# Kernel tuning notes

Hardware: AMD Instinct MI355X
Metric: run time of the kernel (lower is better)

Reference implementation:

```python
import jax, jax.numpy as jnp
import numpy as np

N_NODES = 100000
N_EDGES = 1600000
D_IN, D_H, D_OUT = 128, 128, 64


def gcn_conv(x, src, dst, W, b, n_nodes):
    """PyG GCNConv (eval): x' = D^{-1/2} (A+I) D^{-1/2} X W + b.
    src/dst already include self-loops."""
    h = x @ W  # [N, d_out] -- transform first (fewer FLOPs when d_out <= d_in)
    deg = jax.ops.segment_sum(jnp.ones_like(dst, dtype=h.dtype), dst, num_segments=n_nodes)
    dinv = jnp.where(deg > 0, jax.lax.rsqrt(deg), 0.0)
    norm = dinv[src] * dinv[dst]  # [E]
    msg = h[src] * norm[:, None]  # gather + scale
    out = jax.ops.segment_sum(msg, dst, num_segments=n_nodes)  # scatter-add
    return out + b


def setup_inputs() -> dict:
    key = jax.random.key(0)
    k = jax.random.split(key, 8)
    x = jax.random.normal(k[0], (N_NODES, D_IN), dtype=jnp.float32)
    edge_index = jax.random.randint(k[1], (2, N_EDGES), 0, N_NODES, dtype=jnp.int32)
    s = 0.1
    W1 = jax.random.normal(k[2], (D_IN, D_H), dtype=jnp.float32) * s
    b1 = jnp.zeros((D_H,), dtype=jnp.float32)
    W2 = jax.random.normal(k[3], (D_H, D_H), dtype=jnp.float32) * s
    b2 = jnp.zeros((D_H,), dtype=jnp.float32)
    W3 = jax.random.normal(k[4], (D_H, D_OUT), dtype=jnp.float32) * s
    b3 = jnp.zeros((D_OUT,), dtype=jnp.float32)
    return {"x": x, "edge_index": edge_index, "W1": W1, "b1": b1,
            "W2": W2, "b2": b2, "W3": W3, "b3": b3}


def reference(x, edge_index, W1, b1, W2, b2, W3, b3):
    n = x.shape[0]
    # add self-loops once (shared by all layers)
    loops = jnp.arange(n, dtype=edge_index.dtype)
    src = jnp.concatenate([edge_index[0], loops])
    dst = jnp.concatenate([edge_index[1], loops])
    h = gcn_conv(x, src, dst, W1, b1, n)
    h = jax.nn.relu(h)  # dropout = identity in eval mode
    h = gcn_conv(h, src, dst, W2, b2, n)
    h = jax.nn.relu(h)
    out = gcn_conv(h, src, dst, W3, b3, n)
    return out
```

## Files before the change

kernel.cpp:

```cpp
#include <hip/hip_runtime.h>
#include <hip/hip_fp16.h>

#define N_NODES 100000
#define N_EDGES 1600000
#define NBUCKET 196
#define CAP     8960
#define EPB     6250

typedef _Float16 half8 __attribute__((ext_vector_type(8)));
typedef float float4v __attribute__((ext_vector_type(4)));

__launch_bounds__(256)
__global__ void k_partition(const int* __restrict__ src, const int* __restrict__ dst,
                            int* __restrict__ bcur, int2* __restrict__ ebuf, int E) {
    __shared__ int hist[200];
    __shared__ int basebkt[200];
    const int tid = threadIdx.x;
    if (tid < 200) hist[tid] = 0;
    __syncthreads();
    const int e0 = blockIdx.x * EPB, e1 = min(e0 + EPB, E);
    for (int e = e0 + tid; e < e1; e += 256) atomicAdd(&hist[dst[e] >> 9], 1);
    __syncthreads();
    if (tid < NBUCKET) {
        int h = hist[tid];
        basebkt[tid] = tid * CAP + (h ? atomicAdd(&bcur[tid], h) : 0);
    }
    __syncthreads();
    if (tid < 200) hist[tid] = 0;
    __syncthreads();
    for (int e = e0 + tid; e < e1; e += 256) {
        int d = dst[e];
        int bk = d >> 9;
        int o = atomicAdd(&hist[bk], 1);
        ebuf[basebkt[bk] + o] = make_int2(src[e], d);
    }
}

__launch_bounds__(256)
__global__ void k_bsort(const int2* __restrict__ ebuf, const int* __restrict__ bcur,
                        int* __restrict__ adj, int* __restrict__ stv,
                        int* __restrict__ deg, float* __restrict__ dinv, int N) {
    __shared__ int cnt[512];
    __shared__ int offs[512];
    const int b = blockIdx.x;
    const int tid = threadIdx.x;
    const int base = b * CAP;
    const int n_b = min(bcur[b], CAP);
    const int node0 = b << 9;
    cnt[tid] = 0; cnt[tid + 256] = 0;
    __syncthreads();
    for (int i = tid; i < n_b; i += 256) {
        unsigned local = (unsigned)(ebuf[base + i].y - node0);
        if (local < 512u) atomicAdd(&cnt[local], 1);
    }
    __syncthreads();
    if (tid < 64) {
        int v[8], tot = 0;
#pragma unroll
        for (int j = 0; j < 8; ++j) { int t = cnt[tid * 8 + j]; v[j] = tot; tot += t; }
        int inc = tot;
#pragma unroll
        for (int d = 1; d < 64; d <<= 1) {
            int u = __shfl_up(inc, d, 64);
            if (tid >= d) inc += u;
        }
        const int excl = inc - tot;
#pragma unroll
        for (int j = 0; j < 8; ++j) offs[tid * 8 + j] = excl + v[j];
    }
    __syncthreads();
#pragma unroll
    for (int h = 0; h < 2; ++h) {
        int local = tid + h * 256;
        int node = node0 + local;
        if (node < N) {
            stv[node] = base + offs[local];
            deg[node] = cnt[local];
            dinv[node] = rsqrtf((float)(cnt[local] + 1));
        }
    }
    __syncthreads();
    for (int i = tid; i < n_b; i += 256) {
        int2 e = ebuf[base + i];
        unsigned local = (unsigned)(e.y - node0);
        if (local < 512u) {
            int pos = atomicAdd(&offs[local], 1);
            adj[base + pos] = e.x;
        }
    }
}

__global__ void k_wswz_all(const float* __restrict__ W1, const float* __restrict__ W2,
                           const float* __restrict__ W3, _Float16* __restrict__ wz1,
                           _Float16* __restrict__ wz2, _Float16* __restrict__ wz3) {
    int t = blockIdx.x * 256 + threadIdx.x;
    const float* W; _Float16* wsz; int BN;
    if (t < 2048)      { W = W1; wsz = wz1; BN = 128; }
    else if (t < 4096) { W = W2; wsz = wz2; BN = 128; t -= 2048; }
    else if (t < 5120) { W = W3; wsz = wz3; BN = 64;  t -= 4096; }
    else return;
    const int l = t & 63;
    const int kblk = (t >> 6) & 3;
    const int nt = t >> 8;
    const int krow = kblk * 32 + ((l >> 4) << 3);
    const int col = nt * 16 + (l & 15);
    _Float16 v[8];
#pragma unroll
    for (int j = 0; j < 8; ++j) v[j] = (_Float16)W[(krow + j) * BN + col];
    *(uint4*)&wsz[t << 3] = *(uint4*)v;
}

template <int BN, bool AFP16>
__launch_bounds__(256, 4)
__global__ void k_gemm_mfma(const void* __restrict__ Xv, const _Float16* __restrict__ wsz,
                            const float* __restrict__ dinv, __half* __restrict__ out, int N) {
    constexpr int NT = BN / 16;
    constexpr int PAD = 8;
    __shared__ __align__(16) _Float16 smem[BN * 128];

    const int tid = threadIdx.x;
    for (int i = tid; i < BN * 16; i += 256)
        *(uint4*)&smem[i << 3] = *(const uint4*)&wsz[i << 3];

    const int w = tid >> 6;
    const int lane = tid & 63;
    const int q = lane >> 4;
    const int m = lane & 15;
    const int row0 = blockIdx.x * 64;
    const int arow = row0 + w * 16 + m;
    const int arowc = arow < N ? arow : N - 1;

    float4v acc[NT];
#pragma unroll
    for (int nt = 0; nt < NT; ++nt) acc[nt] = (float4v){0.f, 0.f, 0.f, 0.f};

    __syncthreads();

#pragma unroll
    for (int kblk = 0; kblk < 4; ++kblk) {
        half8 af;
        if constexpr (AFP16) {
            const _Float16* A = (const _Float16*)Xv + (size_t)arowc * 128 + (q << 3);
            af = *(const half8*)(A + kblk * 32);
        } else {
            const float* A = (const float*)Xv + (size_t)arowc * 128 + (q << 3);
            float4 a0 = *(const float4*)(A + kblk * 32);
            float4 a1 = *(const float4*)(A + kblk * 32 + 4);
            af[0] = (_Float16)a0.x; af[1] = (_Float16)a0.y;
            af[2] = (_Float16)a0.z; af[3] = (_Float16)a0.w;
            af[4] = (_Float16)a1.x; af[5] = (_Float16)a1.y;
            af[6] = (_Float16)a1.z; af[7] = (_Float16)a1.w;
        }
#pragma unroll
        for (int nt = 0; nt < NT; ++nt) {
            half8 bf = *(const half8*)&smem[(((nt << 2) + kblk) << 9) + (lane << 3)];
            acc[nt] = __builtin_amdgcn_mfma_f32_16x16x32_f16(af, bf, acc[nt], 0, 0, 0);
        }
    }

    float s[4];
#pragma unroll
    for (int r = 0; r < 4; ++r) {
        int rr = row0 + w * 16 + q * 4 + r;
        s[r] = dinv[rr < N ? rr : N - 1];
    }
    __syncthreads();
    _Float16* eb = smem;
#pragma unroll
    for (int nt = 0; nt < NT; ++nt)
#pragma unroll
        for (int r = 0; r < 4; ++r)
            eb[(w * 16 + q * 4 + r) * (BN + PAD) + nt * 16 + m] = (_Float16)(acc[nt][r] * s[r]);
    __syncthreads();
    constexpr int CPR = BN / 8;
    for (int i = tid; i < 64 * CPR; i += 256) {
        int row = i / CPR;
        int cf = (i % CPR) * 8;
        if (row0 + row < N)
            *(uint4*)&out[(size_t)(row0 + row) * BN + cf] = *(uint4*)&eb[row * (BN + PAD) + cf];
    }
}

template <int D, bool RELU, typename OT>
__launch_bounds__(256)
__global__ void k_agg(const __half* __restrict__ tp, const int* __restrict__ adj,
                      const int* __restrict__ startv, const int* __restrict__ deg,
                      const float* __restrict__ dinv, const float* __restrict__ b,
                      OT* __restrict__ out, int N) {
    const int node = (blockIdx.x << 2) + (threadIdx.x >> 6);
    const int lane = threadIdx.x & 63;
    if (node >= N) return;
    const int s = startv[node];
    const int cnt = deg[node];
    const float di = dinv[node];

    if constexpr (D == 128) {
        const __half2* t2 = (const __half2*)tp;
        float2 acc = __half22float2(t2[(size_t)node * 64 + lane]);
        int e = 0;
        for (; e + 8 <= cnt; e += 8) {
            int j[8];
#pragma unroll
            for (int u = 0; u < 8; ++u) j[u] = adj[s + e + u];
            __half2 r[8];
#pragma unroll
            for (int u = 0; u < 8; ++u) r[u] = t2[(size_t)j[u] * 64 + lane];
#pragma unroll
            for (int u = 0; u < 8; ++u) {
                float2 f = __half22float2(r[u]);
                acc.x += f.x; acc.y += f.y;
            }
        }
        for (; e < cnt; ++e) {
            float2 f = __half22float2(t2[(size_t)adj[s + e] * 64 + lane]);
            acc.x += f.x; acc.y += f.y;
        }
        float2 bb = ((const float2*)b)[lane];
        float o0 = di * acc.x + bb.x;
        float o1 = di * acc.y + bb.y;
        if (RELU) { o0 = fmaxf(o0, 0.f); o1 = fmaxf(o1, 0.f); }
        ((__half2*)out)[(size_t)node * 64 + lane] = __floats2half2_rn(o0, o1);
    } else {
        float acc = __half2float(tp[(size_t)node * 64 + lane]);
        int e = 0;
        for (; e + 8 <= cnt; e += 8) {
            int j[8];
#pragma unroll
            for (int u = 0; u < 8; ++u) j[u] = adj[s + e + u];
            __half r[8];
#pragma unroll
            for (int u = 0; u < 8; ++u) r[u] = tp[(size_t)j[u] * 64 + lane];
#pragma unroll
            for (int u = 0; u < 8; ++u) acc += __half2float(r[u]);
        }
        for (; e < cnt; ++e) acc += __half2float(tp[(size_t)adj[s + e] * 64 + lane]);
        float o = di * acc + b[lane];
        if (RELU) o = fmaxf(o, 0.f);
        out[(size_t)node * 64 + lane] = (OT)o;
    }
}

extern "C" void kernel_launch(void* const* d_in, const int* in_sizes, int n_in,
                              void* d_out, int out_size, void* d_ws, size_t ws_size,
                              hipStream_t stream) {
    const float* x  = (const float*)d_in[0];
    const int*   ei = (const int*)d_in[1];
    const float* W1 = (const float*)d_in[2];
    const float* b1 = (const float*)d_in[3];
    const float* W2 = (const float*)d_in[4];
    const float* b2 = (const float*)d_in[5];
    const float* W3 = (const float*)d_in[6];
    const float* b3 = (const float*)d_in[7];
    float* out = (float*)d_out;
    const int* src = ei;
    const int* dst = ei + N_EDGES;

    char* p = (char*)d_ws;
    __half* tp      = (__half*)p;    p += (size_t)N_NODES * 128 * 2;
    _Float16* hbuf  = (_Float16*)p;  p += (size_t)N_NODES * 128 * 2;
    int*   deg  = (int*)p;    p += (size_t)N_NODES * 4;
    float* dinv = (float*)p;  p += (size_t)N_NODES * 4;
    int*   stv  = (int*)p;    p += (size_t)N_NODES * 4;
    int*   bCur = (int*)p;    p += 1024;
    int*   adj  = (int*)p;    p += (size_t)NBUCKET * CAP * 4 + 16384;
    _Float16* wz1 = (_Float16*)p; p += 16384 * 2;
    _Float16* wz2 = (_Float16*)p; p += 16384 * 2;
    _Float16* wz3 = (_Float16*)p; p += 8192 * 2;
    size_t need = (size_t)(p - (char*)d_ws);
    if (ws_size < need) return;

    int2* ebuf = (int2*)tp;

    hipMemsetAsync(bCur, 0, 1024, stream);

    k_wswz_all<<<20, 256, 0, stream>>>(W1, W2, W3, wz1, wz2, wz3);
    k_partition<<<256, 256, 0, stream>>>(src, dst, bCur, ebuf, N_EDGES);
    k_bsort<<<NBUCKET, 256, 0, stream>>>(ebuf, bCur, adj, stv, deg, dinv, N_NODES);

    const int gb = (N_NODES + 63) / 64;
    const int ab = (N_NODES + 3) / 4;
    k_gemm_mfma<128, false><<<gb, 256, 0, stream>>>(x, wz1, dinv, tp, N_NODES);
    k_agg<128, true, _Float16><<<ab, 256, 0, stream>>>(tp, adj, stv, deg, dinv, b1, hbuf, N_NODES);
    k_gemm_mfma<128, true><<<gb, 256, 0, stream>>>(hbuf, wz2, dinv, tp, N_NODES);
    k_agg<128, true, _Float16><<<ab, 256, 0, stream>>>(tp, adj, stv, deg, dinv, b2, hbuf, N_NODES);
    k_gemm_mfma<64, true><<<gb, 256, 0, stream>>>(hbuf, wz3, dinv, tp, N_NODES);
    k_agg<64, false, float><<<ab, 256, 0, stream>>>(tp, adj, stv, deg, dinv, b3, out, N_NODES);
}
```

Measured before the change: 402.6 us.

## Pack edges into one int and split 128-wide aggregation into two column halves

The partition pass now packs each edge as (src<<9)|(dst&511) in a single int instead of an int2. This halves the scratch traffic in partition and bucket sort and drops the range check. The 128-wide aggregation is split into two launches, each gathering one 64-column half per node with scalar half loads. The aim is to shrink the gather working set so the table stays resident in cache, at the cost of reading adjacency twice and using narrower 2-byte loads. Packing assumes src < 2^22, which holds for 100k nodes.

```diff
diff --git a/kernel.cpp b/kernel.cpp
--- a/kernel.cpp
+++ b/kernel.cpp
@@ -12,7 +12,7 @@
 
 __launch_bounds__(256)
 __global__ void k_partition(const int* __restrict__ src, const int* __restrict__ dst,
-                            int* __restrict__ bcur, int2* __restrict__ ebuf, int E) {
+                            int* __restrict__ bcur, int* __restrict__ ebuf, int E) {
     __shared__ int hist[200];
     __shared__ int basebkt[200];
     const int tid = threadIdx.x;
@@ -32,12 +32,12 @@
         int d = dst[e];
         int bk = d >> 9;
         int o = atomicAdd(&hist[bk], 1);
-        ebuf[basebkt[bk] + o] = make_int2(src[e], d);
-    }
-}
-
-__launch_bounds__(256)
-__global__ void k_bsort(const int2* __restrict__ ebuf, const int* __restrict__ bcur,
+        ebuf[basebkt[bk] + o] = (src[e] << 9) | (d & 511);
+    }
+}
+
+__launch_bounds__(256)
+__global__ void k_bsort(const int* __restrict__ ebuf, const int* __restrict__ bcur,
                         int* __restrict__ adj, int* __restrict__ stv,
                         int* __restrict__ deg, float* __restrict__ dinv, int N) {
     __shared__ int cnt[512];
@@ -49,10 +49,8 @@
     const int node0 = b << 9;
     cnt[tid] = 0; cnt[tid + 256] = 0;
     __syncthreads();
-    for (int i = tid; i < n_b; i += 256) {
-        unsigned local = (unsigned)(ebuf[base + i].y - node0);
-        if (local < 512u) atomicAdd(&cnt[local], 1);
-    }
+    for (int i = tid; i < n_b; i += 256)
+        atomicAdd(&cnt[ebuf[base + i] & 511], 1);
     __syncthreads();
     if (tid < 64) {
         int v[8], tot = 0;
@@ -81,12 +79,9 @@
     }
     __syncthreads();
     for (int i = tid; i < n_b; i += 256) {
-        int2 e = ebuf[base + i];
-        unsigned local = (unsigned)(e.y - node0);
-        if (local < 512u) {
-            int pos = atomicAdd(&offs[local], 1);
-            adj[base + pos] = e.x;
-        }
+        int pk = ebuf[base + i];
+        int pos = atomicAdd(&offs[pk & 511], 1);
+        adj[base + pos] = pk >> 9;
     }
 }
 
@@ -181,63 +176,65 @@
     }
 }
 
-template <int D, bool RELU, typename OT>
-__launch_bounds__(256)
-__global__ void k_agg(const __half* __restrict__ tp, const int* __restrict__ adj,
-                      const int* __restrict__ startv, const int* __restrict__ deg,
-                      const float* __restrict__ dinv, const float* __restrict__ b,
-                      OT* __restrict__ out, int N) {
+template <bool RELU>
+__launch_bounds__(256)
+__global__ void k_agg_half(const __half* __restrict__ tp, const int* __restrict__ adj,
+                           const int* __restrict__ startv, const int* __restrict__ deg,
+                           const float* __restrict__ dinv, const float* __restrict__ b,
+                           _Float16* __restrict__ out, int N, int h) {
     const int node = (blockIdx.x << 2) + (threadIdx.x >> 6);
     const int lane = threadIdx.x & 63;
     if (node >= N) return;
     const int s = startv[node];
     const int cnt = deg[node];
     const float di = dinv[node];
-
-    if constexpr (D == 128) {
-        const __half2* t2 = (const __half2*)tp;
-        float2 acc = __half22float2(t2[(size_t)node * 64 + lane]);
-        int e = 0;
-        for (; e + 8 <= cnt; e += 8) {
-            int j[8];
-#pragma unroll
-            for (int u = 0; u < 8; ++u) j[u] = adj[s + e + u];
-            __half2 r[8];
-#pragma unroll
-            for (int u = 0; u < 8; ++u) r[u] = t2[(size_t)j[u] * 64 + lane];
-#pragma unroll
-            for (int u = 0; u < 8; ++u) {
-                float2 f = __half22float2(r[u]);
-                acc.x += f.x; acc.y += f.y;
-            }
-        }
-        for (; e < cnt; ++e) {
-            float2 f = __half22float2(t2[(size_t)adj[s + e] * 64 + lane]);
-            acc.x += f.x; acc.y += f.y;
-        }
-        float2 bb = ((const float2*)b)[lane];
-        float o0 = di * acc.x + bb.x;
-        float o1 = di * acc.y + bb.y;
-        if (RELU) { o0 = fmaxf(o0, 0.f); o1 = fmaxf(o1, 0.f); }
-        ((__half2*)out)[(size_t)node * 64 + lane] = __floats2half2_rn(o0, o1);
-    } else {
-        float acc = __half2float(tp[(size_t)node * 64 + lane]);
-        int e = 0;
-        for (; e + 8 <= cnt; e += 8) {
-            int j[8];
-#pragma unroll
-            for (int u = 0; u < 8; ++u) j[u] = adj[s + e + u];
-            __half r[8];
-#pragma unroll
-            for (int u = 0; u < 8; ++u) r[u] = tp[(size_t)j[u] * 64 + lane];
-#pragma unroll
-            for (int u = 0; u < 8; ++u) acc += __half2float(r[u]);
-        }
-        for (; e < cnt; ++e) acc += __half2float(tp[(size_t)adj[s + e] * 64 + lane]);
-        float o = di * acc + b[lane];
-        if (RELU) o = fmaxf(o, 0.f);
-        out[(size_t)node * 64 + lane] = (OT)o;
-    }
+    const __half* col = tp + h * 64 + lane;
+
+    float acc = __half2float(col[(size_t)node * 128]);
+    int e = 0;
+    for (; e + 8 <= cnt; e += 8) {
+        int j[8];
+#pragma unroll
+        for (int u = 0; u < 8; ++u) j[u] = adj[s + e + u];
+        __half r[8];
+#pragma unroll
+        for (int u = 0; u < 8; ++u) r[u] = col[(size_t)j[u] * 128];
+#pragma unroll
+        for (int u = 0; u < 8; ++u) acc += __half2float(r[u]);
+    }
+    for (; e < cnt; ++e) acc += __half2float(col[(size_t)adj[s + e] * 128]);
+    float o = di * acc + b[h * 64 + lane];
+    if (RELU) o = fmaxf(o, 0.f);
+    out[(size_t)node * 128 + h * 64 + lane] = (_Float16)o;
+}
+
+__launch_bounds__(256)
+__global__ void k_agg64(const __half* __restrict__ tp, const int* __restrict__ adj,
+                        const int* __restrict__ startv, const int* __restrict__ deg,
+                        const float* __restrict__ dinv, const float* __restrict__ b,
+                        float* __restrict__ out, int N) {
+    const int node = (blockIdx.x << 2) + (threadIdx.x >> 6);
+    const int lane = threadIdx.x & 63;
+    if (node >= N) return;
+    const int s = startv[node];
+    const int cnt = deg[node];
+    const float di = dinv[node];
+
+    float acc = __half2float(tp[(size_t)node * 64 + lane]);
+    int e = 0;
+    for (; e + 8 <= cnt; e += 8) {
+        int j[8];
+#pragma unroll
+        for (int u = 0; u < 8; ++u) j[u] = adj[s + e + u];
+        __half r[8];
+#pragma unroll
+        for (int u = 0; u < 8; ++u) r[u] = tp[(size_t)j[u] * 64 + lane];
+#pragma unroll
+        for (int u = 0; u < 8; ++u) acc += __half2float(r[u]);
+    }
+    for (; e < cnt; ++e) acc += __half2float(tp[(size_t)adj[s + e] * 64 + lane]);
+    float o = di * acc + b[lane];
+    out[(size_t)node * 64 + lane] = o;
 }
 
 extern "C" void kernel_launch(void* const* d_in, const int* in_sizes, int n_in,
@@ -269,7 +266,7 @@
     size_t need = (size_t)(p - (char*)d_ws);
     if (ws_size < need) return;
 
-    int2* ebuf = (int2*)tp;
+    int* ebuf = (int*)tp;
 
     hipMemsetAsync(bCur, 0, 1024, stream);
 
@@ -280,9 +277,11 @@
     const int gb = (N_NODES + 63) / 64;
     const int ab = (N_NODES + 3) / 4;
     k_gemm_mfma<128, false><<<gb, 256, 0, stream>>>(x, wz1, dinv, tp, N_NODES);
-    k_agg<128, true, _Float16><<<ab, 256, 0, stream>>>(tp, adj, stv, deg, dinv, b1, hbuf, N_NODES);
+    k_agg_half<true><<<ab, 256, 0, stream>>>(tp, adj, stv, deg, dinv, b1, hbuf, N_NODES, 0);
+    k_agg_half<true><<<ab, 256, 0, stream>>>(tp, adj, stv, deg, dinv, b1, hbuf, N_NODES, 1);
     k_gemm_mfma<128, true><<<gb, 256, 0, stream>>>(hbuf, wz2, dinv, tp, N_NODES);
-    k_agg<128, true, _Float16><<<ab, 256, 0, stream>>>(tp, adj, stv, deg, dinv, b2, hbuf, N_NODES);
+    k_agg_half<true><<<ab, 256, 0, stream>>>(tp, adj, stv, deg, dinv, b2, hbuf, N_NODES, 0);
+    k_agg_half<true><<<ab, 256, 0, stream>>>(tp, adj, stv, deg, dinv, b2, hbuf, N_NODES, 1);
     k_gemm_mfma<64, true><<<gb, 256, 0, stream>>>(hbuf, wz3, dinv, tp, N_NODES);
-    k_agg<64, false, float><<<ab, 256, 0, stream>>>(tp, adj, stv, deg, dinv, b3, out, N_NODES);
-}
+    k_agg64<<<ab, 256, 0, stream>>>(tp, adj, stv, deg, dinv, b3, out, N_NODES);
+}
```

Result: slower. 508.4 us (+26.3%).
